# Performance work log

Measured on AMD Instinct MI355X. Metric: run time of the kernel, lower is better.

## Reference

```python
import jax, jax.numpy as jnp
import numpy as np


def setup_inputs() -> dict:
    key = jax.random.key(0)
    k0, k1, k2, k3 = jax.random.split(key, 4)
    T, H, I, E = 2048, 2048, 5632, 8
    return {
        "hidden_states": jax.random.normal(k0, (T, H), dtype=jnp.float32),
        "gate_w": jax.random.normal(k1, (E, H), dtype=jnp.float32) * 0.02,
        "w1": jax.random.normal(k2, (E, 2 * I, H), dtype=jnp.float32) * 0.02,
        "w2": jax.random.normal(k3, (E, H, I), dtype=jnp.float32) * 0.02,
        "top_k": 2,
    }


def reference(hidden_states, gate_w, w1, w2, top_k):
    # hidden_states: [T, H]; gate_w: [E, H]; w1: [E, 2I, H]; w2: [E, H, I]
    T = hidden_states.shape[0]
    E = w1.shape[0]
    router_logits = hidden_states @ gate_w.T                    # [T, E]
    probs = jax.nn.softmax(router_logits, axis=-1)
    topk_w, topk_idx = jax.lax.top_k(probs, top_k)              # [T, k]
    # renormalize=False in fused_moe: use raw softmax top-k weights.
    # Dense combine matrix C[t, e] = weight of expert e for token t (0 if unrouted).
    combine = jnp.zeros((T, E), dtype=probs.dtype)
    combine = combine.at[jnp.arange(T)[:, None], topk_idx].add(topk_w)
    out = jnp.zeros_like(hidden_states)
    for e in range(E):  # small fixed expert loop
        gate_up = hidden_states @ w1[e].T                       # [T, 2I]
        g, u = jnp.split(gate_up, 2, axis=-1)
        h = jax.nn.silu(g) * u                                  # SiluAndMul
        out = out + combine[:, e:e + 1] * (h @ w2[e].T)         # [T, H]
    return out
```

## Files before the change

### kernel.cpp

```cpp
#include <hip/hip_runtime.h>
#include <hip/hip_bf16.h>

typedef __bf16 bf16_t;
typedef __bf16 bf16x8 __attribute__((ext_vector_type(8)));
typedef float  f32x4  __attribute__((ext_vector_type(4)));

constexpr int T_ = 2048, H_ = 2048, I_ = 5632, E_ = 8, S_ = T_ * 2;

constexpr size_t OFF_HB    = 0;
constexpr size_t OFF_HOUT  = OFF_HB    + (size_t)T_ * H_ * 2;
constexpr size_t OFF_DPART = OFF_HOUT  + (size_t)S_ * I_ * 2;
constexpr size_t OFF_TOS   = OFF_DPART + (size_t)S_ * H_ * 4;
constexpr size_t OFF_SOT   = OFF_TOS   + (size_t)S_ * 4;
constexpr size_t OFF_TKI   = OFF_SOT   + (size_t)S_ * 4;
constexpr size_t OFF_TKW   = OFF_TKI   + (size_t)S_ * 4;
constexpr size_t OFF_CNT   = OFF_TKW   + (size_t)S_ * 4;
constexpr size_t OFF_OFFS  = OFF_CNT   + 64;
constexpr size_t OFF_CUR   = OFF_OFFS  + 64;

__device__ __forceinline__ void gload16(const void* g, void* l) {
  __builtin_amdgcn_global_load_lds(
      (const __attribute__((address_space(1))) void*)g,
      (__attribute__((address_space(3))) void*)l, 16, 0, 0);
}

__device__ __forceinline__ bf16x8 cvt8(f32x4 a, f32x4 b) {
  bf16x8 r;
  r[0]=(bf16_t)a[0]; r[1]=(bf16_t)a[1]; r[2]=(bf16_t)a[2]; r[3]=(bf16_t)a[3];
  r[4]=(bf16_t)b[0]; r[5]=(bf16_t)b[1]; r[6]=(bf16_t)b[2]; r[7]=(bf16_t)b[3];
  return r;
}

__global__ __launch_bounds__(256)
void router_kernel(const float* __restrict__ hs, const float* __restrict__ gw,
                   int* __restrict__ tki, float* __restrict__ tkw,
                   int* __restrict__ counts, bf16_t* __restrict__ hb)
{
  const int t = blockIdx.x;
  const int tid = threadIdx.x;
  const int lane = tid & 63, wid = tid >> 6;
  const float* hrow = hs + (size_t)t * H_;
  const int c0 = tid * 8;
  float4 h0 = *(const float4*)(hrow + c0);
  float4 h1 = *(const float4*)(hrow + c0 + 4);
  bf16x8 hv;
  hv[0]=(bf16_t)h0.x; hv[1]=(bf16_t)h0.y; hv[2]=(bf16_t)h0.z; hv[3]=(bf16_t)h0.w;
  hv[4]=(bf16_t)h1.x; hv[5]=(bf16_t)h1.y; hv[6]=(bf16_t)h1.z; hv[7]=(bf16_t)h1.w;
  *(bf16x8*)(hb + (size_t)t * H_ + c0) = hv;

  float acc[E_];
  #pragma unroll
  for (int e = 0; e < E_; ++e) {
    const float* g = gw + (size_t)e * H_ + c0;
    float4 g0 = *(const float4*)(g);
    float4 g1 = *(const float4*)(g + 4);
    acc[e] = h0.x*g0.x + h0.y*g0.y + h0.z*g0.z + h0.w*g0.w
           + h1.x*g1.x + h1.y*g1.y + h1.z*g1.z + h1.w*g1.w;
  }
  #pragma unroll
  for (int e = 0; e < E_; ++e)
    #pragma unroll
    for (int o = 32; o > 0; o >>= 1)
      acc[e] += __shfl_down(acc[e], o);
  __shared__ float red[4][E_];
  if (lane == 0)
    #pragma unroll
    for (int e = 0; e < E_; ++e) red[wid][e] = acc[e];
  __syncthreads();
  if (tid == 0) {
    float l[E_];
    #pragma unroll
    for (int e = 0; e < E_; ++e) l[e] = red[0][e] + red[1][e] + red[2][e] + red[3][e];
    float m = l[0];
    #pragma unroll
    for (int e = 1; e < E_; ++e) m = fmaxf(m, l[e]);
    float p[E_]; float s = 0.f;
    #pragma unroll
    for (int e = 0; e < E_; ++e) { p[e] = __expf(l[e] - m); s += p[e]; }
    int i1 = 0;
    #pragma unroll
    for (int e = 1; e < E_; ++e) if (l[e] > l[i1]) i1 = e;
    int i2 = (i1 == 0) ? 1 : 0;
    #pragma unroll
    for (int e = 0; e < E_; ++e) if (e != i1 && l[e] > l[i2]) i2 = e;
    tki[2*t] = i1; tki[2*t+1] = i2;
    tkw[2*t] = p[i1] / s; tkw[2*t+1] = p[i2] / s;
    atomicAdd(&counts[i1], 1);
    atomicAdd(&counts[i2], 1);
  }
}

__global__ void scan_kernel(const int* __restrict__ counts, const int* __restrict__ tki,
                            int* __restrict__ offs, int* __restrict__ cursor,
                            int* __restrict__ tos, int* __restrict__ sot)
{
  if (threadIdx.x == 0) {
    int run = 0;
    for (int e = 0; e < E_; ++e) { offs[e] = run; cursor[e] = run; run += counts[e]; }
  }
  __syncthreads();
  for (int t = threadIdx.x; t < T_; t += blockDim.x) {
    #pragma unroll
    for (int k = 0; k < 2; ++k) {
      int e = tki[2*t + k];
      int s = atomicAdd(&cursor[e], 1);
      tos[s] = t;
      sot[2*t + k] = s;
    }
  }
}

constexpr int G1_BM = 128, G1_BN = 64, G1_BK = 32;
constexpr int G1_BUF = G1_BM * G1_BK * 2 + 2 * G1_BN * G1_BK * 4;

__global__ __launch_bounds__(256, 2)
void gemm1_kernel(const bf16_t* __restrict__ hb, const float* __restrict__ w1,
                  const int* __restrict__ tos, const int* __restrict__ offs,
                  const int* __restrict__ counts, bf16_t* __restrict__ hout)
{
  const int bid = blockIdx.x;
  const int e   = bid & 7;
  const int idx = bid >> 3;
  const int mt  = idx & 15;
  const int nt  = idx >> 4;

  const int cnt = counts[e];
  const int m0 = mt * G1_BM;
  if (m0 >= cnt) return;
  const int off = offs[e];
  const int n0 = nt * G1_BN;

  const float* Wg = w1 + (size_t)e * (2 * (size_t)I_ * H_) + (size_t)n0 * H_;

  __shared__ char smem[3 * G1_BUF];

  const int tid = threadIdx.x;
  const int lane = tid & 63, wid = tid >> 6;
  const int wm = wid >> 1, wn = wid & 1;
  const int l15 = lane & 15, l4 = lane >> 4;

  const bf16_t* agp[2]; int aoff[2];
  #pragma unroll
  for (int i = 0; i < 2; ++i) {
    int q = wid * 2 + i;
    int row = q * 16 + (lane >> 2);
    int slot = off + m0 + row, mx = off + cnt - 1;
    if (slot > mx) slot = mx;
    agp[i]  = hb + (size_t)tos[slot] * H_ + ((lane & 3) ^ ((lane >> 3) & 3)) * 8;
    aoff[i] = q * 1024;
  }
  const float* bgp[4]; int boff[4];
  #pragma unroll
  for (int i = 0; i < 4; ++i) {
    int q = wid * 4 + i;
    int lrow = q * 8 + (lane >> 3);
    size_t wr = (lrow < 64) ? (size_t)lrow : (size_t)(I_ - 64 + lrow);
    bgp[i]  = Wg + wr * H_ + ((lane & 7) ^ ((lane >> 3) & 7)) * 4;
    boff[i] = q * 1024;
  }

  auto stage = [&](int b, int t) {
    char* ab = smem + b * G1_BUF;
    char* bb = ab + 8192;
    const int k0 = t * G1_BK;
    #pragma unroll
    for (int i = 0; i < 2; ++i) gload16(agp[i] + k0, ab + aoff[i]);
    #pragma unroll
    for (int i = 0; i < 4; ++i) gload16(bgp[i] + k0, bb + boff[i]);
  };

  f32x4 accg[4][2], accu[4][2];
  #pragma unroll
  for (int mi = 0; mi < 4; ++mi)
    #pragma unroll
    for (int ni = 0; ni < 2; ++ni) {
      accg[mi][ni] = f32x4{0.f,0.f,0.f,0.f};
      accu[mi][ni] = f32x4{0.f,0.f,0.f,0.f};
    }

  auto compute = [&](int b) {
    const char* ab = smem + b * G1_BUF;
    const char* bb = ab + 8192;
    bf16x8 af[4], bgf[2], buf2[2];
    const int as = (l4 ^ ((l15 >> 1) & 3)) * 16;
    #pragma unroll
    for (int mi = 0; mi < 4; ++mi) {
      int r = wm * 64 + mi * 16 + l15;
      af[mi] = *(const bf16x8*)(ab + r * 64 + as);
    }
    const int s0 = ((2 * l4) ^ (l15 & 7)) * 16;
    #pragma unroll
    for (int ni = 0; ni < 2; ++ni) {
      int rg = wn * 32 + ni * 16 + l15;
      const char* rowg = bb + rg * 128;
      const char* rowu = bb + (rg + 64) * 128;
      f32x4 g0 = *(const f32x4*)(rowg + s0);
      f32x4 g1 = *(const f32x4*)(rowg + (s0 ^ 16));
      f32x4 u0 = *(const f32x4*)(rowu + s0);
      f32x4 u1 = *(const f32x4*)(rowu + (s0 ^ 16));
      bgf[ni]  = cvt8(g0, g1);
      buf2[ni] = cvt8(u0, u1);
    }
    #pragma unroll
    for (int mi = 0; mi < 4; ++mi)
      #pragma unroll
      for (int ni = 0; ni < 2; ++ni) {
        accg[mi][ni] = __builtin_amdgcn_mfma_f32_16x16x32_bf16(af[mi], bgf[ni],  accg[mi][ni], 0, 0, 0);
        accu[mi][ni] = __builtin_amdgcn_mfma_f32_16x16x32_bf16(af[mi], buf2[ni], accu[mi][ni], 0, 0, 0);
      }
  };

  constexpr int NK = H_ / G1_BK;
  stage(0, 0); stage(1, 1);
  int bs = 2, bc = 0;
  for (int t = 0; t < NK - 2; ++t) {
    __builtin_amdgcn_s_barrier();
    stage(bs, t + 2);
    asm volatile("s_waitcnt vmcnt(12)" ::: "memory");
    __builtin_amdgcn_s_barrier();
    __builtin_amdgcn_sched_barrier(0);
    compute(bc);
    bs = (bs == 2) ? 0 : bs + 1;
    bc = (bc == 2) ? 0 : bc + 1;
  }
  __builtin_amdgcn_s_barrier();
  asm volatile("s_waitcnt vmcnt(6)" ::: "memory");
  __builtin_amdgcn_s_barrier();
  __builtin_amdgcn_sched_barrier(0);
  compute(bc);
  bc = (bc == 2) ? 0 : bc + 1;
  __builtin_amdgcn_s_barrier();
  asm volatile("s_waitcnt vmcnt(0)" ::: "memory");
  __builtin_amdgcn_s_barrier();
  __builtin_amdgcn_sched_barrier(0);
  compute(bc);

  #pragma unroll
  for (int mi = 0; mi < 4; ++mi)
    #pragma unroll
    for (int ni = 0; ni < 2; ++ni)
      #pragma unroll
      for (int j = 0; j < 4; ++j) {
        int rel = wm*64 + mi*16 + l4*4 + j;
        if (m0 + rel < cnt) {
          int col = n0 + wn*32 + ni*16 + l15;
          float g = accg[mi][ni][j];
          float u = accu[mi][ni][j];
          float hvv = (g / (1.0f + __expf(-g))) * u;
          hout[(size_t)(off + m0 + rel) * I_ + col] = (bf16_t)hvv;
        }
      }
}

constexpr int G2_BM = 128, G2_BN = 128, G2_BK = 32;
constexpr int G2_BUF = G2_BM * G2_BK * 2 + G2_BN * G2_BK * 4;

__global__ __launch_bounds__(256, 2)
void gemm2_kernel(const bf16_t* __restrict__ hbuf, const float* __restrict__ w2,
                  const int* __restrict__ offs, const int* __restrict__ counts,
                  float* __restrict__ dpart)
{
  const int bid = blockIdx.x;
  const int e   = bid & 7;
  const int idx = bid >> 3;
  const int mt  = idx & 15;
  const int nt  = idx >> 4;

  const int cnt = counts[e];
  const int m0 = mt * G2_BM;
  if (m0 >= cnt) return;
  const int off = offs[e];
  const int n0 = nt * G2_BN;
  const float* W = w2 + (size_t)e * ((size_t)H_ * I_) + (size_t)n0 * I_;

  __shared__ char smem[3 * G2_BUF];

  const int tid = threadIdx.x;
  const int lane = tid & 63, wid = tid >> 6;
  const int wm = wid >> 1, wn = wid & 1;
  const int l15 = lane & 15, l4 = lane >> 4;

  const bf16_t* agp[2]; int aoff[2];
  #pragma unroll
  for (int i = 0; i < 2; ++i) {
    int q = wid * 2 + i;
    int row = q * 16 + (lane >> 2);
    int slot = off + m0 + row, mx = off + cnt - 1;
    if (slot > mx) slot = mx;
    agp[i]  = hbuf + (size_t)slot * I_ + ((lane & 3) ^ ((lane >> 3) & 3)) * 8;
    aoff[i] = q * 1024;
  }
  const float* bgp[4]; int boff[4];
  #pragma unroll
  for (int i = 0; i < 4; ++i) {
    int q = wid * 4 + i;
    int lrow = q * 8 + (lane >> 3);
    bgp[i]  = W + (size_t)lrow * I_ + ((lane & 7) ^ ((lane >> 3) & 7)) * 4;
    boff[i] = q * 1024;
  }

  auto stage = [&](int b, int t) {
    char* ab = smem + b * G2_BUF;
    char* bb = ab + 8192;
    const int k0 = t * G2_BK;
    #pragma unroll
    for (int i = 0; i < 2; ++i) gload16(agp[i] + k0, ab + aoff[i]);
    #pragma unroll
    for (int i = 0; i < 4; ++i) gload16(bgp[i] + k0, bb + boff[i]);
  };

  f32x4 acc[4][4];
  #pragma unroll
  for (int mi = 0; mi < 4; ++mi)
    #pragma unroll
    for (int ni = 0; ni < 4; ++ni) acc[mi][ni] = f32x4{0.f,0.f,0.f,0.f};

  auto compute = [&](int b) {
    const char* ab = smem + b * G2_BUF;
    const char* bb = ab + 8192;
    bf16x8 af[4], bf[4];
    const int as = (l4 ^ ((l15 >> 1) & 3)) * 16;
    #pragma unroll
    for (int mi = 0; mi < 4; ++mi) {
      int r = wm * 64 + mi * 16 + l15;
      af[mi] = *(const bf16x8*)(ab + r * 64 + as);
    }
    const int s0 = ((2 * l4) ^ (l15 & 7)) * 16;
    #pragma unroll
    for (int ni = 0; ni < 4; ++ni) {
      int r = wn * 64 + ni * 16 + l15;
      const char* row = bb + r * 128;
      f32x4 b0 = *(const f32x4*)(row + s0);
      f32x4 b1 = *(const f32x4*)(row + (s0 ^ 16));
      bf[ni] = cvt8(b0, b1);
    }
    #pragma unroll
    for (int mi = 0; mi < 4; ++mi)
      #pragma unroll
      for (int ni = 0; ni < 4; ++ni)
        acc[mi][ni] = __builtin_amdgcn_mfma_f32_16x16x32_bf16(af[mi], bf[ni], acc[mi][ni], 0, 0, 0);
  };

  constexpr int NK = I_ / G2_BK;
  stage(0, 0); stage(1, 1);
  int bs = 2, bc = 0;
  for (int t = 0; t < NK - 2; ++t) {
    __builtin_amdgcn_s_barrier();
    stage(bs, t + 2);
    asm volatile("s_waitcnt vmcnt(12)" ::: "memory");
    __builtin_amdgcn_s_barrier();
    __builtin_amdgcn_sched_barrier(0);
    compute(bc);
    bs = (bs == 2) ? 0 : bs + 1;
    bc = (bc == 2) ? 0 : bc + 1;
  }
  __builtin_amdgcn_s_barrier();
  asm volatile("s_waitcnt vmcnt(6)" ::: "memory");
  __builtin_amdgcn_s_barrier();
  __builtin_amdgcn_sched_barrier(0);
  compute(bc);
  bc = (bc == 2) ? 0 : bc + 1;
  __builtin_amdgcn_s_barrier();
  asm volatile("s_waitcnt vmcnt(0)" ::: "memory");
  __builtin_amdgcn_s_barrier();
  __builtin_amdgcn_sched_barrier(0);
  compute(bc);

  #pragma unroll
  for (int mi = 0; mi < 4; ++mi)
    #pragma unroll
    for (int ni = 0; ni < 4; ++ni)
      #pragma unroll
      for (int j = 0; j < 4; ++j) {
        int rel = wm*64 + mi*16 + l4*4 + j;
        if (m0 + rel < cnt) {
          int col = n0 + wn*64 + ni*16 + l15;
          dpart[(size_t)(off + m0 + rel) * H_ + col] = acc[mi][ni][j];
        }
      }
}

__global__ __launch_bounds__(256)
void combine_kernel(const float* __restrict__ dpart, const int* __restrict__ sot,
                    const float* __restrict__ tkw, float* __restrict__ out)
{
  int idx = blockIdx.x * 256 + threadIdx.x;
  int t = idx >> 9;
  int c = (idx & 511) * 4;
  float wA = tkw[2*t], wB = tkw[2*t+1];
  int sA = sot[2*t], sB = sot[2*t+1];
  float4 a = *(const float4*)(dpart + (size_t)sA * H_ + c);
  float4 b = *(const float4*)(dpart + (size_t)sB * H_ + c);
  float4 o;
  o.x = wA*a.x + wB*b.x; o.y = wA*a.y + wB*b.y;
  o.z = wA*a.z + wB*b.z; o.w = wA*a.w + wB*b.w;
  *(float4*)(out + (size_t)t * H_ + c) = o;
}

extern "C" void kernel_launch(void* const* d_in, const int* in_sizes, int n_in,
                              void* d_out, int out_size, void* d_ws, size_t ws_size,
                              hipStream_t stream) {
  const float* hs = (const float*)d_in[0];
  const float* gw = (const float*)d_in[1];
  const float* w1 = (const float*)d_in[2];
  const float* w2 = (const float*)d_in[3];
  float* out = (float*)d_out;
  char* ws = (char*)d_ws;

  bf16_t* hb    = (bf16_t*)(ws + OFF_HB);
  bf16_t* hout  = (bf16_t*)(ws + OFF_HOUT);
  float*  dpart = (float*) (ws + OFF_DPART);
  int*    tos   = (int*)   (ws + OFF_TOS);
  int*    sot   = (int*)   (ws + OFF_SOT);
  int*    tki   = (int*)   (ws + OFF_TKI);
  float*  tkw   = (float*) (ws + OFF_TKW);
  int*    cnt   = (int*)   (ws + OFF_CNT);
  int*    offp  = (int*)   (ws + OFF_OFFS);
  int*    curp  = (int*)   (ws + OFF_CUR);

  hipMemsetAsync(ws + OFF_CNT, 0, 64, stream);

  router_kernel<<<T_, 256, 0, stream>>>(hs, gw, tki, tkw, cnt, hb);
  scan_kernel<<<1, 256, 0, stream>>>(cnt, tki, offp, curp, tos, sot);
  gemm1_kernel<<<(T_ / G1_BM) * (I_ / G1_BN) * E_, 256, 0, stream>>>(hb, w1, tos, offp, cnt, hout);
  gemm2_kernel<<<(T_ / G2_BM) * (H_ / G2_BN) * E_, 256, 0, stream>>>(hout, w2, offp, cnt, dpart);
  combine_kernel<<<(T_ * H_ / 4) / 256, 256, 0, stream>>>(dpart, sot, tkw, out);
}
```

Baseline: 849.3 us.

## Switch GEMMs to double-buffered LDS with new A swizzle and higher occupancy

Both grouped GEMM kernels move from a 3-stage LDS ring with explicit vmcnt waits to a simple 2-stage double buffer synchronized by __syncthreads. The LDS footprint per block drops, so launch bounds rise to 3 blocks per CU for more occupancy. The A tile layout is also re-swizzled, packing two 64-byte rows into each 128-byte LDS row, to avoid bank conflicts on the fragment reads. The cost is a shallower prefetch depth and a full barrier every K step, which can expose global-load latency, and a 3-block launch bound may limit registers for the large accumulator sets.

```diff
diff --git a/kernel.cpp b/kernel.cpp
--- a/kernel.cpp
+++ b/kernel.cpp
@@ -111,9 +111,9 @@
 }
 
 constexpr int G1_BM = 128, G1_BN = 64, G1_BK = 32;
-constexpr int G1_BUF = G1_BM * G1_BK * 2 + 2 * G1_BN * G1_BK * 4;
-
-__global__ __launch_bounds__(256, 2)
+constexpr int G1_BUF = 8192 + 16384;
+
+__global__ __launch_bounds__(256, 3)
 void gemm1_kernel(const bf16_t* __restrict__ hb, const float* __restrict__ w1,
                   const int* __restrict__ tos, const int* __restrict__ offs,
                   const int* __restrict__ counts, bf16_t* __restrict__ hout)
@@ -132,7 +132,7 @@
 
   const float* Wg = w1 + (size_t)e * (2 * (size_t)I_ * H_) + (size_t)n0 * H_;
 
-  __shared__ char smem[3 * G1_BUF];
+  __shared__ char smem[2 * G1_BUF];
 
   const int tid = threadIdx.x;
   const int lane = tid & 63, wid = tid >> 6;
@@ -143,19 +143,22 @@
   #pragma unroll
   for (int i = 0; i < 2; ++i) {
     int q = wid * 2 + i;
-    int row = q * 16 + (lane >> 2);
+    int rp = q * 8 + (lane >> 3);
+    int w  = (lane & 7) ^ (rp & 7);
+    int row = 2 * rp + (w >> 2);
     int slot = off + m0 + row, mx = off + cnt - 1;
     if (slot > mx) slot = mx;
-    agp[i]  = hb + (size_t)tos[slot] * H_ + ((lane & 3) ^ ((lane >> 3) & 3)) * 8;
+    agp[i]  = hb + (size_t)tos[slot] * H_ + (w & 3) * 8;
     aoff[i] = q * 1024;
   }
   const float* bgp[4]; int boff[4];
   #pragma unroll
   for (int i = 0; i < 4; ++i) {
     int q = wid * 4 + i;
-    int lrow = q * 8 + (lane >> 3);
-    size_t wr = (lrow < 64) ? (size_t)lrow : (size_t)(I_ - 64 + lrow);
-    bgp[i]  = Wg + wr * H_ + ((lane & 7) ^ ((lane >> 3) & 7)) * 4;
+    int row = q * 8 + (lane >> 3);
+    int w   = (lane & 7) ^ (row & 7);
+    size_t wr = (row < 64) ? (size_t)row : (size_t)(I_ - 64 + row);
+    bgp[i]  = Wg + wr * H_ + w * 4;
     boff[i] = q * 1024;
   }
 
@@ -178,26 +181,28 @@
       accu[mi][ni] = f32x4{0.f,0.f,0.f,0.f};
     }
 
+  const int physA = ((((l15 & 1) << 2) | l4) ^ ((l15 >> 1) & 7)) * 16;
+  const int aro   = (l15 >> 1);
+  const int pB0   = (((2 * l4) ^ (l15 & 7))) * 16;
+
   auto compute = [&](int b) {
     const char* ab = smem + b * G1_BUF;
     const char* bb = ab + 8192;
     bf16x8 af[4], bgf[2], buf2[2];
-    const int as = (l4 ^ ((l15 >> 1) & 3)) * 16;
     #pragma unroll
     for (int mi = 0; mi < 4; ++mi) {
-      int r = wm * 64 + mi * 16 + l15;
-      af[mi] = *(const bf16x8*)(ab + r * 64 + as);
-    }
-    const int s0 = ((2 * l4) ^ (l15 & 7)) * 16;
+      int rp = wm * 32 + mi * 8 + aro;
+      af[mi] = *(const bf16x8*)(ab + rp * 128 + physA);
+    }
     #pragma unroll
     for (int ni = 0; ni < 2; ++ni) {
       int rg = wn * 32 + ni * 16 + l15;
       const char* rowg = bb + rg * 128;
       const char* rowu = bb + (rg + 64) * 128;
-      f32x4 g0 = *(const f32x4*)(rowg + s0);
-      f32x4 g1 = *(const f32x4*)(rowg + (s0 ^ 16));
-      f32x4 u0 = *(const f32x4*)(rowu + s0);
-      f32x4 u1 = *(const f32x4*)(rowu + (s0 ^ 16));
+      f32x4 g0 = *(const f32x4*)(rowg + pB0);
+      f32x4 g1 = *(const f32x4*)(rowg + (pB0 ^ 16));
+      f32x4 u0 = *(const f32x4*)(rowu + pB0);
+      f32x4 u1 = *(const f32x4*)(rowu + (pB0 ^ 16));
       bgf[ni]  = cvt8(g0, g1);
       buf2[ni] = cvt8(u0, u1);
     }
@@ -211,29 +216,15 @@
   };
 
   constexpr int NK = H_ / G1_BK;
-  stage(0, 0); stage(1, 1);
-  int bs = 2, bc = 0;
-  for (int t = 0; t < NK - 2; ++t) {
-    __builtin_amdgcn_s_barrier();
-    stage(bs, t + 2);
-    asm volatile("s_waitcnt vmcnt(12)" ::: "memory");
-    __builtin_amdgcn_s_barrier();
-    __builtin_amdgcn_sched_barrier(0);
-    compute(bc);
-    bs = (bs == 2) ? 0 : bs + 1;
-    bc = (bc == 2) ? 0 : bc + 1;
-  }
-  __builtin_amdgcn_s_barrier();
-  asm volatile("s_waitcnt vmcnt(6)" ::: "memory");
-  __builtin_amdgcn_s_barrier();
-  __builtin_amdgcn_sched_barrier(0);
-  compute(bc);
-  bc = (bc == 2) ? 0 : bc + 1;
-  __builtin_amdgcn_s_barrier();
-  asm volatile("s_waitcnt vmcnt(0)" ::: "memory");
-  __builtin_amdgcn_s_barrier();
-  __builtin_amdgcn_sched_barrier(0);
-  compute(bc);
+  stage(0, 0);
+  __syncthreads();
+  int cur = 0;
+  for (int t = 0; t < NK; ++t) {
+    if (t + 1 < NK) stage(cur ^ 1, t + 1);
+    compute(cur);
+    __syncthreads();
+    cur ^= 1;
+  }
 
   #pragma unroll
   for (int mi = 0; mi < 4; ++mi)
@@ -253,9 +244,9 @@
 }
 
 constexpr int G2_BM = 128, G2_BN = 128, G2_BK = 32;
-constexpr int G2_BUF = G2_BM * G2_BK * 2 + G2_BN * G2_BK * 4;
-
-__global__ __launch_bounds__(256, 2)
+constexpr int G2_BUF = 8192 + 16384;
+
+__global__ __launch_bounds__(256, 3)
 void gemm2_kernel(const bf16_t* __restrict__ hbuf, const float* __restrict__ w2,
                   const int* __restrict__ offs, const int* __restrict__ counts,
                   float* __restrict__ dpart)
@@ -273,7 +264,7 @@
   const int n0 = nt * G2_BN;
   const float* W = w2 + (size_t)e * ((size_t)H_ * I_) + (size_t)n0 * I_;
 
-  __shared__ char smem[3 * G2_BUF];
+  __shared__ char smem[2 * G2_BUF];
 
   const int tid = threadIdx.x;
   const int lane = tid & 63, wid = tid >> 6;
@@ -284,18 +275,21 @@
   #pragma unroll
   for (int i = 0; i < 2; ++i) {
     int q = wid * 2 + i;
-    int row = q * 16 + (lane >> 2);
+    int rp = q * 8 + (lane >> 3);
+    int w  = (lane & 7) ^ (rp & 7);
+    int row = 2 * rp + (w >> 2);
     int slot = off + m0 + row, mx = off + cnt - 1;
     if (slot > mx) slot = mx;
-    agp[i]  = hbuf + (size_t)slot * I_ + ((lane & 3) ^ ((lane >> 3) & 3)) * 8;
+    agp[i]  = hbuf + (size_t)slot * I_ + (w & 3) * 8;
     aoff[i] = q * 1024;
   }
   const float* bgp[4]; int boff[4];
   #pragma unroll
   for (int i = 0; i < 4; ++i) {
     int q = wid * 4 + i;
-    int lrow = q * 8 + (lane >> 3);
-    bgp[i]  = W + (size_t)lrow * I_ + ((lane & 7) ^ ((lane >> 3) & 7)) * 4;
+    int row = q * 8 + (lane >> 3);
+    int w   = (lane & 7) ^ (row & 7);
+    bgp[i]  = W + (size_t)row * I_ + w * 4;
     boff[i] = q * 1024;
   }
 
@@ -315,23 +309,25 @@
     #pragma unroll
     for (int ni = 0; ni < 4; ++ni) acc[mi][ni] = f32x4{0.f,0.f,0.f,0.f};
 
+  const int physA = ((((l15 & 1) << 2) | l4) ^ ((l15 >> 1) & 7)) * 16;
+  const int aro   = (l15 >> 1);
+  const int pB0   = (((2 * l4) ^ (l15 & 7))) * 16;
+
   auto compute = [&](int b) {
     const char* ab = smem + b * G2_BUF;
     const char* bb = ab + 8192;
     bf16x8 af[4], bf[4];
-    const int as = (l4 ^ ((l15 >> 1) & 3)) * 16;
     #pragma unroll
     for (int mi = 0; mi < 4; ++mi) {
-      int r = wm * 64 + mi * 16 + l15;
-      af[mi] = *(const bf16x8*)(ab + r * 64 + as);
-    }
-    const int s0 = ((2 * l4) ^ (l15 & 7)) * 16;
+      int rp = wm * 32 + mi * 8 + aro;
+      af[mi] = *(const bf16x8*)(ab + rp * 128 + physA);
+    }
     #pragma unroll
     for (int ni = 0; ni < 4; ++ni) {
       int r = wn * 64 + ni * 16 + l15;
-      const char* row = bb + r * 128;
-      f32x4 b0 = *(const f32x4*)(row + s0);
-      f32x4 b1 = *(const f32x4*)(row + (s0 ^ 16));
+      const char* rowb = bb + r * 128;
+      f32x4 b0 = *(const f32x4*)(rowb + pB0);
+      f32x4 b1 = *(const f32x4*)(rowb + (pB0 ^ 16));
       bf[ni] = cvt8(b0, b1);
     }
     #pragma unroll
@@ -342,29 +338,15 @@
   };
 
   constexpr int NK = I_ / G2_BK;
-  stage(0, 0); stage(1, 1);
-  int bs = 2, bc = 0;
-  for (int t = 0; t < NK - 2; ++t) {
-    __builtin_amdgcn_s_barrier();
-    stage(bs, t + 2);
-    asm volatile("s_waitcnt vmcnt(12)" ::: "memory");
-    __builtin_amdgcn_s_barrier();
-    __builtin_amdgcn_sched_barrier(0);
-    compute(bc);
-    bs = (bs == 2) ? 0 : bs + 1;
-    bc = (bc == 2) ? 0 : bc + 1;
-  }
-  __builtin_amdgcn_s_barrier();
-  asm volatile("s_waitcnt vmcnt(6)" ::: "memory");
-  __builtin_amdgcn_s_barrier();
-  __builtin_amdgcn_sched_barrier(0);
-  compute(bc);
-  bc = (bc == 2) ? 0 : bc + 1;
-  __builtin_amdgcn_s_barrier();
-  asm volatile("s_waitcnt vmcnt(0)" ::: "memory");
-  __builtin_amdgcn_s_barrier();
-  __builtin_amdgcn_sched_barrier(0);
-  compute(bc);
+  stage(0, 0);
+  __syncthreads();
+  int cur = 0;
+  for (int t = 0; t < NK; ++t) {
+    if (t + 1 < NK) stage(cur ^ 1, t + 1);
+    compute(cur);
+    __syncthreads();
+    cur ^= 1;
+  }
 
   #pragma unroll
   for (int mi = 0; mi < 4; ++mi)
```

After: 905.2 us. 6.6% more time.
